# Kernel tuning notes

Measured on AMD Instinct MI355X. Metric: run time of the kernel, lower is better.

## Reference

```python
import jax, jax.numpy as jnp
import numpy as np

B, S, D_IN, HID, H = 4, 2048, 1024, 1024, 16
DH = HID // H


def setup_inputs() -> dict:
    key = jax.random.key(0)
    ks = jax.random.split(key, 10)
    s = 0.02
    return {
        "x": jax.random.normal(ks[0], (B, S, D_IN), dtype=jnp.float32),
        "Wq": jax.random.normal(ks[1], (D_IN, HID), dtype=jnp.float32) * s,
        "bq": jnp.zeros((HID,), dtype=jnp.float32),
        "Wk": jax.random.normal(ks[2], (D_IN, HID), dtype=jnp.float32) * s,
        "bk": jnp.zeros((HID,), dtype=jnp.float32),
        "Wv": jax.random.normal(ks[3], (D_IN, HID), dtype=jnp.float32) * s,
        "bv": jnp.zeros((HID,), dtype=jnp.float32),
        "Wo": jax.random.normal(ks[4], (HID, HID), dtype=jnp.float32) * s,
        "bo": jnp.zeros((HID,), dtype=jnp.float32),
        "padding_mask": jax.random.randint(ks[5], (B, S), 0, 2, dtype=jnp.int32),
    }


def reference(x, Wq, bq, Wk, bk, Wv, bv, Wo, bo, padding_mask):
    b, s, _ = x.shape
    q = (x @ Wq + bq).reshape(b, s, H, DH)  # [b, s, h, dh]
    k = (x @ Wk + bk).reshape(b, s, H, DH)
    v = (x @ Wv + bv).reshape(b, s, H, DH)

    # ALiBi: symmetric |i-j| distance bias, per-head slopes 2^{-m}
    r = jnp.arange(s)
    pos = jnp.abs(r[None, :] - r[:, None]).astype(jnp.float32)  # [s, s]
    step = 8.0 / H
    slopes = jnp.power(2.0, -jnp.arange(step, 8.0 + step, step, dtype=jnp.float32))  # [h]
    alibi = slopes[:, None, None] * pos[None, :, :]  # [h, s, s]

    scale = jnp.sqrt(jnp.float32(DH))
    attn = jnp.einsum("bqhd,bkhd->bhqk", q, k)
    attn = (attn - alibi[None]) / scale
    attn = jnp.where(padding_mask[:, None, None, :] == 0, -jnp.inf, attn)
    p = jax.nn.softmax(attn, axis=-1)

    out = jnp.einsum("bhqk,bkhd->bqhd", p, v).reshape(b, s, HID)
    return out @ Wo + bo
```

## Files before the change

### kernel.cpp

```cpp
#include <hip/hip_runtime.h>
#include <stdint.h>

#define NB     4
#define SEQ    2048
#define NH     16
#define DHD    64
#define DM     1024
#define MTOT   (NB*SEQ)

typedef __attribute__((ext_vector_type(8))) short bf16x8;
typedef __attribute__((ext_vector_type(4))) float f32x4;

__device__ __forceinline__ short f2bf(float f) {
  uint32_t u = __float_as_uint(f);
  u = (u + 0x7FFFu + ((u >> 16) & 1u)) >> 16;
  return (short)u;
}

__device__ __forceinline__ uint32_t cvtpk(float lo, float hi) {
  uint32_t r;
  asm("v_cvt_pk_bf16_f32 %0, %1, %2" : "=v"(r) : "v"(lo), "v"(hi));
  return r;
}

__device__ __forceinline__ float exp2a(float x) {
  float r;
  asm("v_exp_f32 %0, %1" : "=v"(r) : "v"(x));
  return r;
}

__device__ __forceinline__ float max3f(float a, float b, float c) {
  return fmaxf(fmaxf(a, b), c);
}

__device__ __forceinline__ f32x4 mfma16(bf16x8 a, bf16x8 b, f32x4 c) {
  return __builtin_amdgcn_mfma_f32_16x16x32_bf16(a, b, c, 0, 0, 0);
}

__device__ __forceinline__ void async16(const void* g, void* l) {
  __builtin_amdgcn_global_load_lds(
      (const __attribute__((address_space(1))) void*)g,
      (__attribute__((address_space(3))) void*)l, 16, 0, 0);
}

__global__ void k_cast(const float* __restrict__ in, short* __restrict__ out, int n) {
  int i = (blockIdx.x * blockDim.x + threadIdx.x) * 8;
  if (i >= n) return;
  float4 a = *reinterpret_cast<const float4*>(in + i);
  float4 b = *reinterpret_cast<const float4*>(in + i + 4);
  bf16x8 v;
  v[0] = f2bf(a.x); v[1] = f2bf(a.y); v[2] = f2bf(a.z); v[3] = f2bf(a.w);
  v[4] = f2bf(b.x); v[5] = f2bf(b.y); v[6] = f2bf(b.z); v[7] = f2bf(b.w);
  *reinterpret_cast<bf16x8*>(out + i) = v;
}

__global__ void k_maskbias(const int* __restrict__ pm, float* __restrict__ fb, int n) {
  int i = blockIdx.x * blockDim.x + threadIdx.x;
  if (i < n) fb[i] = pm[i] ? 0.0f : -1e30f;
}

__global__ void k_transpose(const float* __restrict__ in, short* __restrict__ out) {
  __shared__ float tile[32][33];
  int n0 = blockIdx.x * 32, k0 = blockIdx.y * 32;
  int tx = threadIdx.x, ty = threadIdx.y;
  #pragma unroll
  for (int i = 0; i < 32; i += 8)
    tile[ty + i][tx] = in[(size_t)(k0 + ty + i) * DM + n0 + tx];
  __syncthreads();
  #pragma unroll
  for (int i = 0; i < 32; i += 8)
    out[(size_t)(n0 + ty + i) * DM + k0 + tx] = f2bf(tile[tx][ty + i]);
}

template<int MODE>
__global__ void __launch_bounds__(256) k_gemm(const short* __restrict__ A,
                                              const short* __restrict__ Bt,
                                              const float* __restrict__ bias,
                                              void* __restrict__ Cv, float scale) {
  __shared__ short lA[128 * 32];
  __shared__ short lB[128 * 32];
  int lin = blockIdx.y * gridDim.x + blockIdx.x;
  int s = ((lin & 7) << 6) | (lin >> 3);
  int m0 = (s & 63) * 128, n0 = (s >> 6) * 128;
  int tid = threadIdx.x, lane = tid & 63, w = tid >> 6;
  int wr = w >> 1, wc = w & 1;
  int l15 = lane & 15, lg = lane >> 4;
  f32x4 acc[4][4] = {};

  int r0 = tid >> 2, c0 = (tid & 3) * 8;
  int r1 = (tid + 256) >> 2, c1 = ((tid + 256) & 3) * 8;
  const short* ga0 = A + (size_t)(m0 + r0) * DM + c0;
  const short* ga1 = A + (size_t)(m0 + r1) * DM + c1;
  const short* gb0 = Bt + (size_t)(n0 + r0) * DM + c0;
  const short* gb1 = Bt + (size_t)(n0 + r1) * DM + c1;
  short* lA0 = lA + w * 512;
  short* lA1 = lA + 2048 + w * 512;
  short* lB0 = lB + w * 512;
  short* lB1 = lB + 2048 + w * 512;

  for (int k0 = 0; k0 < DM; k0 += 32) {
    async16(ga0 + k0, lA0);
    async16(ga1 + k0, lA1);
    async16(gb0 + k0, lB0);
    async16(gb1 + k0, lB1);
    __syncthreads();
    bf16x8 af[4], bfr[4];
    #pragma unroll
    for (int i = 0; i < 4; ++i) {
      af[i]  = *reinterpret_cast<const bf16x8*>(lA + (wr * 64 + i * 16 + l15) * 32 + lg * 8);
      bfr[i] = *reinterpret_cast<const bf16x8*>(lB + (wc * 64 + i * 16 + l15) * 32 + lg * 8);
    }
    #pragma unroll
    for (int i = 0; i < 4; ++i)
      #pragma unroll
      for (int j = 0; j < 4; ++j)
        acc[i][j] = mfma16(af[i], bfr[j], acc[i][j]);
    __syncthreads();
  }

  #pragma unroll
  for (int j = 0; j < 4; ++j) {
    int cg = n0 + wc * 64 + j * 16 + l15;
    float bv = bias[cg];
    #pragma unroll
    for (int i = 0; i < 4; ++i) {
      #pragma unroll
      for (int r = 0; r < 4; ++r) {
        int rg = m0 + wr * 64 + i * 16 + lg * 4 + r;
        float val = (acc[i][j][r] + bv) * scale;
        if (MODE == 0)
          ((short*)Cv)[(size_t)rg * DM + cg] = f2bf(val);
        else if (MODE == 1)
          ((short*)Cv)[((size_t)((rg >> 11) * DM + cg)) * SEQ + (rg & 2047)] = f2bf(val);
        else
          ((float*)Cv)[(size_t)rg * DM + cg] = val;
      }
    }
  }
}

__device__ __forceinline__ void softmax_half(const f32x4* st, const float4* fb4,
                                             float c2, float d0, int lg,
                                             float& mrun, float& ssum,
                                             f32x4* acc, uint32_t* wb) {
  float l[16];
  #pragma unroll
  for (int t = 0; t < 4; ++t) {
    l[t * 4 + 0] = fmaf(-c2, fabsf(d0 - (float)(t * 16 + 0)), st[t][0] + fb4[t].x);
    l[t * 4 + 1] = fmaf(-c2, fabsf(d0 - (float)(t * 16 + 1)), st[t][1] + fb4[t].y);
    l[t * 4 + 2] = fmaf(-c2, fabsf(d0 - (float)(t * 16 + 2)), st[t][2] + fb4[t].z);
    l[t * 4 + 3] = fmaf(-c2, fabsf(d0 - (float)(t * 16 + 3)), st[t][3] + fb4[t].w);
  }
  float ma = max3f(l[0], l[1], l[2]);
  float mb = max3f(l[3], l[4], l[5]);
  float mc = max3f(l[6], l[7], l[8]);
  float md = max3f(l[9], l[10], l[11]);
  float me = max3f(l[12], l[13], l[14]);
  float tmax = fmaxf(max3f(ma, mb, mc), max3f(md, me, l[15]));
  tmax = fmaxf(tmax, __shfl_xor(tmax, 16));
  tmax = fmaxf(tmax, __shfl_xor(tmax, 32));

  if (!__all(tmax <= mrun + 8.0f)) {
    float mn = fmaxf(mrun, tmax);
    float fsc = exp2a(mrun - mn);
    mrun = mn;
    ssum *= fsc;
    #pragma unroll
    for (int td = 0; td < 4; ++td) acc[td] *= fsc;
  }

  float p[16];
  #pragma unroll
  for (int i = 0; i < 16; ++i) p[i] = exp2a(l[i] - mrun);
  float a0 = p[0] + p[1],  a1 = p[2] + p[3],  a2 = p[4] + p[5],  a3 = p[6] + p[7];
  float a4 = p[8] + p[9],  a5 = p[10] + p[11], a6 = p[12] + p[13], a7 = p[14] + p[15];
  float b0 = a0 + a1, b1 = a2 + a3, b2 = a4 + a5, b3 = a6 + a7;
  float rs = (b0 + b1) + (b2 + b3);
  rs += __shfl_xor(rs, 16);
  rs += __shfl_xor(rs, 32);
  ssum += rs;

  #pragma unroll
  for (int t = 0; t < 4; ++t) {
    uint2 wv = { cvtpk(p[t * 4 + 0], p[t * 4 + 1]), cvtpk(p[t * 4 + 2], p[t * 4 + 3]) };
    *reinterpret_cast<uint2*>(wb + t * 8 + lg * 2) = wv;
  }
}

__global__ void __launch_bounds__(256, 4) k_attn(const short* __restrict__ Q,
                                                 const short* __restrict__ Kb,
                                                 const short* __restrict__ Vt,
                                                 const float* __restrict__ fbias,
                                                 short* __restrict__ O) {
  __shared__ short lK[64 * 64];
  __shared__ short lV[64 * 64];
  __shared__ uint32_t pbuf[4 * 2 * 16 * 36];
  int qt = blockIdx.x, bh = blockIdx.y;
  int b = bh >> 4, h = bh & 15;
  int tid = threadIdx.x, lane = tid & 63, w = tid >> 6;
  int l15 = lane & 15, lg = lane >> 4;
  int q0 = qt * 128 + w * 32;
  float c2 = exp2f(-0.5f * (float)(h + 1)) * 0.125f * 1.44269504f;

  const short* qpA = Q + (size_t)(b * SEQ + q0 + l15) * DM + h * DHD + lg * 8;
  bf16x8 bqA0 = *reinterpret_cast<const bf16x8*>(qpA);
  bf16x8 bqA1 = *reinterpret_cast<const bf16x8*>(qpA + 32);
  const short* qpB = qpA + (size_t)16 * DM;
  bf16x8 bqB0 = *reinterpret_cast<const bf16x8*>(qpB);
  bf16x8 bqB1 = *reinterpret_cast<const bf16x8*>(qpB + 32);

  int srow0 = w * 8 + (lane >> 3);
  int srow1 = srow0 + 32;
  int sc0 = (lane & 7) ^ (srow0 & 7);
  int sc1 = (lane & 7) ^ (srow1 & 7);
  const short* kg0 = Kb + (size_t)(b * SEQ + srow0) * DM + h * DHD + sc0 * 8;
  const short* kg1 = Kb + (size_t)(b * SEQ + srow1) * DM + h * DHD + sc1 * 8;
  const short* vg0 = Vt + ((size_t)bh * DHD + srow0) * SEQ + sc0 * 8;
  const short* vg1 = Vt + ((size_t)bh * DHD + srow1) * SEQ + sc1 * 8;
  short* dK0 = lK + w * 512;
  short* dK1 = lK + 2048 + w * 512;
  short* dV0 = lV + w * 512;
  short* dV1 = lV + 2048 + w * 512;

  const float* fb = fbias + b * SEQ;
  uint32_t* wbA = pbuf + w * 1152 + l15 * 36;
  uint32_t* wbB = wbA + 576;
  int sw = l15 & 7;

  float mrunA = -1e30f, ssumA = 0.0f, mrunB = -1e30f, ssumB = 0.0f;
  f32x4 accA[4] = {}, accB[4] = {};
  float d0A = (float)(q0 + l15) - (float)(lg * 4);
  float d0B = d0A + 16.0f;

  for (int kt = 0; kt < SEQ; kt += 64) {
    async16(kg0, dK0);
    async16(kg1, dK1);
    async16(vg0, dV0);
    async16(vg1, dV1);
    kg0 += (size_t)64 * DM; kg1 += (size_t)64 * DM; vg0 += 64; vg1 += 64;

    float4 fb4[4];
    #pragma unroll
    for (int t = 0; t < 4; ++t)
      fb4[t] = *reinterpret_cast<const float4*>(fb + kt + t * 16 + lg * 4);

    __syncthreads();

    f32x4 stA[4], stB[4];
    __builtin_amdgcn_s_setprio(1);
    #pragma unroll
    for (int t = 0; t < 4; ++t) {
      int row = t * 16 + l15;
      bf16x8 k0 = *reinterpret_cast<const bf16x8*>(lK + row * 64 + (lg ^ sw) * 8);
      bf16x8 k1 = *reinterpret_cast<const bf16x8*>(lK + row * 64 + ((lg + 4) ^ sw) * 8);
      f32x4 zA = {};
      zA = mfma16(k0, bqA0, zA);
      stA[t] = mfma16(k1, bqA1, zA);
      f32x4 zB = {};
      zB = mfma16(k0, bqB0, zB);
      stB[t] = mfma16(k1, bqB1, zB);
    }
    __builtin_amdgcn_s_setprio(0);

    softmax_half(stA, fb4, c2, d0A, lg, mrunA, ssumA, accA, wbA);
    softmax_half(stB, fb4, c2, d0B, lg, mrunB, ssumB, accB, wbB);

    asm volatile("s_waitcnt lgkmcnt(0)" ::: "memory");
    __builtin_amdgcn_sched_barrier(0);

    __builtin_amdgcn_s_setprio(1);
    #pragma unroll
    for (int ks = 0; ks < 2; ++ks) {
      int t = ks * 2 + (lg >> 1);
      bf16x8 pfA = *reinterpret_cast<const bf16x8*>(wbA + t * 8 + (lg & 1) * 4);
      bf16x8 pfB = *reinterpret_cast<const bf16x8*>(wbB + t * 8 + (lg & 1) * 4);
      #pragma unroll
      for (int td = 0; td < 4; ++td) {
        int row = td * 16 + l15;
        bf16x8 vf = *reinterpret_cast<const bf16x8*>(lV + row * 64 + ((ks * 4 + lg) ^ sw) * 8);
        accA[td] = mfma16(vf, pfA, accA[td]);
        accB[td] = mfma16(vf, pfB, accB[td]);
      }
    }
    __builtin_amdgcn_s_setprio(0);
    d0A -= 64.0f; d0B -= 64.0f;
    __syncthreads();
  }

  float invA = 1.0f / ssumA;
  float invB = 1.0f / ssumB;
  short* opA = O + (size_t)(b * SEQ + q0 + l15) * DM + h * DHD;
  short* opB = opA + (size_t)16 * DM;
  #pragma unroll
  for (int td = 0; td < 4; ++td) {
    uint2 wvA = { cvtpk(accA[td][0] * invA, accA[td][1] * invA),
                  cvtpk(accA[td][2] * invA, accA[td][3] * invA) };
    *reinterpret_cast<uint2*>(opA + td * 16 + lg * 4) = wvA;
    uint2 wvB = { cvtpk(accB[td][0] * invB, accB[td][1] * invB),
                  cvtpk(accB[td][2] * invB, accB[td][3] * invB) };
    *reinterpret_cast<uint2*>(opB + td * 16 + lg * 4) = wvB;
  }
}

extern "C" void kernel_launch(void* const* d_in, const int* in_sizes, int n_in,
                              void* d_out, int out_size, void* d_ws, size_t ws_size,
                              hipStream_t stream) {
  const float* x  = (const float*)d_in[0];
  const float* Wq = (const float*)d_in[1];
  const float* bq = (const float*)d_in[2];
  const float* Wk = (const float*)d_in[3];
  const float* bk = (const float*)d_in[4];
  const float* Wv = (const float*)d_in[5];
  const float* bv = (const float*)d_in[6];
  const float* Wo = (const float*)d_in[7];
  const float* bo = (const float*)d_in[8];
  const int*   pm = (const int*)d_in[9];

  char* ws = (char*)d_ws;
  const size_t MB = 1ull << 20;
  short* xb  = (short*)(ws + 0 * MB);
  short* q   = (short*)(ws + 16 * MB);
  short* k   = (short*)(ws + 32 * MB);
  short* vt  = (short*)(ws + 48 * MB);
  short* ob  = (short*)(ws + 64 * MB);
  short* wqt = (short*)(ws + 80 * MB);
  short* wkt = (short*)(ws + 82 * MB);
  short* wvt = (short*)(ws + 84 * MB);
  short* wot = (short*)(ws + 86 * MB);
  float* fbias = (float*)(ws + 88 * MB);

  k_cast<<<dim3(MTOT * DM / 8 / 256), dim3(256), 0, stream>>>(x, xb, MTOT * DM);
  k_maskbias<<<dim3(MTOT / 256), dim3(256), 0, stream>>>(pm, fbias, MTOT);
  k_transpose<<<dim3(32, 32), dim3(32, 8), 0, stream>>>(Wq, wqt);
  k_transpose<<<dim3(32, 32), dim3(32, 8), 0, stream>>>(Wk, wkt);
  k_transpose<<<dim3(32, 32), dim3(32, 8), 0, stream>>>(Wv, wvt);
  k_transpose<<<dim3(32, 32), dim3(32, 8), 0, stream>>>(Wo, wot);
  k_gemm<0><<<dim3(64, 8), dim3(256), 0, stream>>>(xb, wqt, bq, q, 0.125f * 1.44269504f);
  k_gemm<0><<<dim3(64, 8), dim3(256), 0, stream>>>(xb, wkt, bk, k, 1.0f);
  k_gemm<1><<<dim3(64, 8), dim3(256), 0, stream>>>(xb, wvt, bv, vt, 1.0f);
  k_attn<<<dim3(SEQ / 128, NB * NH), dim3(256), 0, stream>>>(q, k, vt, fbias, ob);
  k_gemm<2><<<dim3(64, 8), dim3(256), 0, stream>>>(ob, wot, bo, d_out, 1.0f);
}
```

Baseline: 283.9 us.

## Register-prefetch next K/V tile during compute and remap attention grid for locality

```diff
diff --git a/kernel.cpp b/kernel.cpp
--- a/kernel.cpp
+++ b/kernel.cpp
@@ -195,7 +195,9 @@
   __shared__ short lK[64 * 64];
   __shared__ short lV[64 * 64];
   __shared__ uint32_t pbuf[4 * 2 * 16 * 36];
-  int qt = blockIdx.x, bh = blockIdx.y;
+  int g = blockIdx.x;
+  int qt = (g >> 3) & 15;
+  int bh = (g & 7) + ((g >> 7) << 3);
   int b = bh >> 4, h = bh & 15;
   int tid = threadIdx.x, lane = tid & 63, w = tid >> 6;
   int l15 = lane & 15, lg = lane >> 4;
@@ -209,18 +211,12 @@
   bf16x8 bqB0 = *reinterpret_cast<const bf16x8*>(qpB);
   bf16x8 bqB1 = *reinterpret_cast<const bf16x8*>(qpB + 32);
 
-  int srow0 = w * 8 + (lane >> 3);
-  int srow1 = srow0 + 32;
-  int sc0 = (lane & 7) ^ (srow0 & 7);
-  int sc1 = (lane & 7) ^ (srow1 & 7);
-  const short* kg0 = Kb + (size_t)(b * SEQ + srow0) * DM + h * DHD + sc0 * 8;
-  const short* kg1 = Kb + (size_t)(b * SEQ + srow1) * DM + h * DHD + sc1 * 8;
-  const short* vg0 = Vt + ((size_t)bh * DHD + srow0) * SEQ + sc0 * 8;
-  const short* vg1 = Vt + ((size_t)bh * DHD + srow1) * SEQ + sc1 * 8;
-  short* dK0 = lK + w * 512;
-  short* dK1 = lK + 2048 + w * 512;
-  short* dV0 = lV + w * 512;
-  short* dV1 = lV + 2048 + w * 512;
+  int srow = tid >> 3;
+  int scol = tid & 7;
+  const short* kgp = Kb + (size_t)(b * SEQ + srow) * DM + h * DHD + scol * 8;
+  const short* vgp = Vt + ((size_t)bh * DHD + srow) * SEQ + scol * 8;
+  int wofs = (scol ^ (srow & 7)) * 8;
+  int kw0 = srow * 64 + wofs, kw1 = kw0 + 32 * 64;
 
   const float* fb = fbias + b * SEQ;
   uint32_t* wbA = pbuf + w * 1152 + l15 * 36;
@@ -232,19 +228,31 @@
   float d0A = (float)(q0 + l15) - (float)(lg * 4);
   float d0B = d0A + 16.0f;
 
+  bf16x8 ks0 = *reinterpret_cast<const bf16x8*>(kgp);
+  bf16x8 ks1 = *reinterpret_cast<const bf16x8*>(kgp + (size_t)32 * DM);
+  bf16x8 vs0 = *reinterpret_cast<const bf16x8*>(vgp);
+  bf16x8 vs1 = *reinterpret_cast<const bf16x8*>(vgp + (size_t)32 * SEQ);
+  kgp += (size_t)64 * DM; vgp += 64;
+  *reinterpret_cast<bf16x8*>(lK + kw0) = ks0;
+  *reinterpret_cast<bf16x8*>(lK + kw1) = ks1;
+  *reinterpret_cast<bf16x8*>(lV + kw0) = vs0;
+  *reinterpret_cast<bf16x8*>(lV + kw1) = vs1;
+  __syncthreads();
+
   for (int kt = 0; kt < SEQ; kt += 64) {
-    async16(kg0, dK0);
-    async16(kg1, dK1);
-    async16(vg0, dV0);
-    async16(vg1, dV1);
-    kg0 += (size_t)64 * DM; kg1 += (size_t)64 * DM; vg0 += 64; vg1 += 64;
+    bool more = (kt + 64) < SEQ;
+    if (more) {
+      ks0 = *reinterpret_cast<const bf16x8*>(kgp);
+      ks1 = *reinterpret_cast<const bf16x8*>(kgp + (size_t)32 * DM);
+      vs0 = *reinterpret_cast<const bf16x8*>(vgp);
+      vs1 = *reinterpret_cast<const bf16x8*>(vgp + (size_t)32 * SEQ);
+      kgp += (size_t)64 * DM; vgp += 64;
+    }
 
     float4 fb4[4];
     #pragma unroll
     for (int t = 0; t < 4; ++t)
       fb4[t] = *reinterpret_cast<const float4*>(fb + kt + t * 16 + lg * 4);
-
-    __syncthreads();
 
     f32x4 stA[4], stB[4];
     __builtin_amdgcn_s_setprio(1);
@@ -284,6 +292,16 @@
     }
     __builtin_amdgcn_s_setprio(0);
     d0A -= 64.0f; d0B -= 64.0f;
+
+    __builtin_amdgcn_s_barrier();
+    __builtin_amdgcn_sched_barrier(0);
+    if (more) {
+      asm volatile("s_waitcnt vmcnt(0)" ::: "memory");
+      *reinterpret_cast<bf16x8*>(lK + kw0) = ks0;
+      *reinterpret_cast<bf16x8*>(lK + kw1) = ks1;
+      *reinterpret_cast<bf16x8*>(lV + kw0) = vs0;
+      *reinterpret_cast<bf16x8*>(lV + kw1) = vs1;
+    }
     __syncthreads();
   }
 
@@ -338,6 +356,6 @@
   k_gemm<0><<<dim3(64, 8), dim3(256), 0, stream>>>(xb, wqt, bq, q, 0.125f * 1.44269504f);
   k_gemm<0><<<dim3(64, 8), dim3(256), 0, stream>>>(xb, wkt, bk, k, 1.0f);
   k_gemm<1><<<dim3(64, 8), dim3(256), 0, stream>>>(xb, wvt, bv, vt, 1.0f);
-  k_attn<<<dim3(SEQ / 128, NB * NH), dim3(256), 0, stream>>>(q, k, vt, fbias, ob);
+  k_attn<<<dim3(SEQ / 128 * NB * NH), dim3(256), 0, stream>>>(q, k, vt, fbias, ob);
   k_gemm<2><<<dim3(64, 8), dim3(256), 0, stream>>>(ob, wot, bo, d_out, 1.0f);
 }
```

After: 317.1 us. 11.7% more time.

## Overlap K/V tile loads with compute via split async prefetch in attention

Applied to the files above, without the earlier changes.

```diff
diff --git a/kernel.cpp b/kernel.cpp
--- a/kernel.cpp
+++ b/kernel.cpp
@@ -187,15 +187,17 @@
   }
 }
 
-__global__ void __launch_bounds__(256, 4) k_attn(const short* __restrict__ Q,
-                                                 const short* __restrict__ Kb,
-                                                 const short* __restrict__ Vt,
-                                                 const float* __restrict__ fbias,
-                                                 short* __restrict__ O) {
+__global__ void __launch_bounds__(256) k_attn(const short* __restrict__ Q,
+                                              const short* __restrict__ Kb,
+                                              const short* __restrict__ Vt,
+                                              const float* __restrict__ fbias,
+                                              short* __restrict__ O) {
   __shared__ short lK[64 * 64];
   __shared__ short lV[64 * 64];
-  __shared__ uint32_t pbuf[4 * 2 * 16 * 36];
-  int qt = blockIdx.x, bh = blockIdx.y;
+  __shared__ uint32_t pbuf[4 * 2 * 16 * 38];
+  int g = blockIdx.x;
+  int qt = (g >> 3) & 15;
+  int bh = (g & 7) + ((g >> 7) << 3);
   int b = bh >> 4, h = bh & 15;
   int tid = threadIdx.x, lane = tid & 63, w = tid >> 6;
   int l15 = lane & 15, lg = lane >> 4;
@@ -223,8 +225,8 @@
   short* dV1 = lV + 2048 + w * 512;
 
   const float* fb = fbias + b * SEQ;
-  uint32_t* wbA = pbuf + w * 1152 + l15 * 36;
-  uint32_t* wbB = wbA + 576;
+  uint32_t* wbA = pbuf + w * 1216 + l15 * 38;
+  uint32_t* wbB = wbA + 608;
   int sw = l15 & 7;
 
   float mrunA = -1e30f, ssumA = 0.0f, mrunB = -1e30f, ssumB = 0.0f;
@@ -232,19 +234,24 @@
   float d0A = (float)(q0 + l15) - (float)(lg * 4);
   float d0B = d0A + 16.0f;
 
+  async16(kg0, dK0);
+  async16(kg1, dK1);
+  kg0 += (size_t)64 * DM; kg1 += (size_t)64 * DM;
+  async16(vg0, dV0);
+  async16(vg1, dV1);
+  vg0 += 64; vg1 += 64;
+
   for (int kt = 0; kt < SEQ; kt += 64) {
-    async16(kg0, dK0);
-    async16(kg1, dK1);
-    async16(vg0, dV0);
-    async16(vg1, dV1);
-    kg0 += (size_t)64 * DM; kg1 += (size_t)64 * DM; vg0 += 64; vg1 += 64;
+    bool more = (kt + 64) < SEQ;
+
+    asm volatile("s_waitcnt vmcnt(2)" ::: "memory");
+    __builtin_amdgcn_s_barrier();
+    __builtin_amdgcn_sched_barrier(0);
 
     float4 fb4[4];
     #pragma unroll
     for (int t = 0; t < 4; ++t)
       fb4[t] = *reinterpret_cast<const float4*>(fb + kt + t * 16 + lg * 4);
-
-    __syncthreads();
 
     f32x4 stA[4], stB[4];
     __builtin_amdgcn_s_setprio(1);
@@ -262,10 +269,23 @@
     }
     __builtin_amdgcn_s_setprio(0);
 
+    __builtin_amdgcn_s_barrier();
+    __builtin_amdgcn_sched_barrier(0);
+    if (more) {
+      async16(kg0, dK0);
+      async16(kg1, dK1);
+      kg0 += (size_t)64 * DM; kg1 += (size_t)64 * DM;
+    }
+
     softmax_half(stA, fb4, c2, d0A, lg, mrunA, ssumA, accA, wbA);
     softmax_half(stB, fb4, c2, d0B, lg, mrunB, ssumB, accB, wbB);
 
     asm volatile("s_waitcnt lgkmcnt(0)" ::: "memory");
+    if (more)
+      asm volatile("s_waitcnt vmcnt(2)" ::: "memory");
+    else
+      asm volatile("s_waitcnt vmcnt(0)" ::: "memory");
+    __builtin_amdgcn_s_barrier();
     __builtin_amdgcn_sched_barrier(0);
 
     __builtin_amdgcn_s_setprio(1);
@@ -284,7 +304,14 @@
     }
     __builtin_amdgcn_s_setprio(0);
     d0A -= 64.0f; d0B -= 64.0f;
-    __syncthreads();
+
+    __builtin_amdgcn_s_barrier();
+    __builtin_amdgcn_sched_barrier(0);
+    if (more) {
+      async16(vg0, dV0);
+      async16(vg1, dV1);
+      vg0 += 64; vg1 += 64;
+    }
   }
 
   float invA = 1.0f / ssumA;
@@ -338,6 +365,6 @@
   k_gemm<0><<<dim3(64, 8), dim3(256), 0, stream>>>(xb, wqt, bq, q, 0.125f * 1.44269504f);
   k_gemm<0><<<dim3(64, 8), dim3(256), 0, stream>>>(xb, wkt, bk, k, 1.0f);
   k_gemm<1><<<dim3(64, 8), dim3(256), 0, stream>>>(xb, wvt, bv, vt, 1.0f);
-  k_attn<<<dim3(SEQ / 128, NB * NH), dim3(256), 0, stream>>>(q, k, vt, fbias, ob);
+  k_attn<<<dim3(SEQ / 128 * NB * NH), dim3(256), 0, stream>>>(q, k, vt, fbias, ob);
   k_gemm<2><<<dim3(64, 8), dim3(256), 0, stream>>>(ob, wot, bo, d_out, 1.0f);
 }
```

After: 322.0 us. 13.4% more time.

## Prepack K/V in MFMA fragment order and load directly from global in single-wave attention

Applied to the files above, without the earlier changes.

```diff
diff --git a/kernel.cpp b/kernel.cpp
--- a/kernel.cpp
+++ b/kernel.cpp
@@ -7,6 +7,7 @@
 #define DHD    64
 #define DM     1024
 #define MTOT   (NB*SEQ)
+#define HSZ    (SEQ*DHD)
 
 typedef __attribute__((ext_vector_type(8))) short bf16x8;
 typedef __attribute__((ext_vector_type(4))) float f32x4;
@@ -128,12 +129,23 @@
       for (int r = 0; r < 4; ++r) {
         int rg = m0 + wr * 64 + i * 16 + lg * 4 + r;
         float val = (acc[i][j][r] + bv) * scale;
-        if (MODE == 0)
+        if (MODE == 0) {
           ((short*)Cv)[(size_t)rg * DM + cg] = f2bf(val);
-        else if (MODE == 1)
-          ((short*)Cv)[((size_t)((rg >> 11) * DM + cg)) * SEQ + (rg & 2047)] = f2bf(val);
-        else
+        } else if (MODE == 1) {
+          int bh2 = ((rg >> 11) << 4) | (cg >> 6);
+          int dh = cg & 63, sl = rg & 2047;
+          size_t fi = (size_t)bh2 * HSZ + (size_t)(sl >> 6) * 4096
+                    + (size_t)((((dh >> 4) * 8 + ((sl >> 3) & 7)) * 16 + (dh & 15)) * 8 + (sl & 7));
+          ((short*)Cv)[fi] = f2bf(val);
+        } else if (MODE == 3) {
+          int bh2 = ((rg >> 11) << 4) | (cg >> 6);
+          int dh = cg & 63, sl = rg & 2047;
+          size_t fi = (size_t)bh2 * HSZ + (size_t)(sl >> 4) * 1024
+                    + (size_t)((((dh >> 3) * 16 + (sl & 15)) * 8) + (dh & 7));
+          ((short*)Cv)[fi] = f2bf(val);
+        } else {
           ((float*)Cv)[(size_t)rg * DM + cg] = val;
+        }
       }
     }
   }
@@ -187,19 +199,19 @@
   }
 }
 
-__global__ void __launch_bounds__(256, 4) k_attn(const short* __restrict__ Q,
-                                                 const short* __restrict__ Kb,
-                                                 const short* __restrict__ Vt,
-                                                 const float* __restrict__ fbias,
-                                                 short* __restrict__ O) {
-  __shared__ short lK[64 * 64];
-  __shared__ short lV[64 * 64];
-  __shared__ uint32_t pbuf[4 * 2 * 16 * 36];
-  int qt = blockIdx.x, bh = blockIdx.y;
+__global__ void __launch_bounds__(64, 3) k_attn(const short* __restrict__ Q,
+                                                const short* __restrict__ KF,
+                                                const short* __restrict__ VF,
+                                                const float* __restrict__ fbias,
+                                                short* __restrict__ O) {
+  __shared__ uint32_t pbuf[2 * 16 * 38];
+  int g = blockIdx.x;
+  int qb = (g >> 3) & 63;
+  int bh = (g & 7) + ((g >> 9) << 3);
   int b = bh >> 4, h = bh & 15;
-  int tid = threadIdx.x, lane = tid & 63, w = tid >> 6;
+  int lane = threadIdx.x;
   int l15 = lane & 15, lg = lane >> 4;
-  int q0 = qt * 128 + w * 32;
+  int q0 = qb * 32;
   float c2 = exp2f(-0.5f * (float)(h + 1)) * 0.125f * 1.44269504f;
 
   const short* qpA = Q + (size_t)(b * SEQ + q0 + l15) * DM + h * DHD + lg * 8;
@@ -209,23 +221,11 @@
   bf16x8 bqB0 = *reinterpret_cast<const bf16x8*>(qpB);
   bf16x8 bqB1 = *reinterpret_cast<const bf16x8*>(qpB + 32);
 
-  int srow0 = w * 8 + (lane >> 3);
-  int srow1 = srow0 + 32;
-  int sc0 = (lane & 7) ^ (srow0 & 7);
-  int sc1 = (lane & 7) ^ (srow1 & 7);
-  const short* kg0 = Kb + (size_t)(b * SEQ + srow0) * DM + h * DHD + sc0 * 8;
-  const short* kg1 = Kb + (size_t)(b * SEQ + srow1) * DM + h * DHD + sc1 * 8;
-  const short* vg0 = Vt + ((size_t)bh * DHD + srow0) * SEQ + sc0 * 8;
-  const short* vg1 = Vt + ((size_t)bh * DHD + srow1) * SEQ + sc1 * 8;
-  short* dK0 = lK + w * 512;
-  short* dK1 = lK + 2048 + w * 512;
-  short* dV0 = lV + w * 512;
-  short* dV1 = lV + 2048 + w * 512;
-
+  const short* kbase = KF + (size_t)bh * HSZ + lane * 8;
+  const short* vbase = VF + (size_t)bh * HSZ + lane * 8;
   const float* fb = fbias + b * SEQ;
-  uint32_t* wbA = pbuf + w * 1152 + l15 * 36;
-  uint32_t* wbB = wbA + 576;
-  int sw = l15 & 7;
+  uint32_t* wbA = pbuf + l15 * 38;
+  uint32_t* wbB = pbuf + 608 + l15 * 38;
 
   float mrunA = -1e30f, ssumA = 0.0f, mrunB = -1e30f, ssumB = 0.0f;
   f32x4 accA[4] = {}, accB[4] = {};
@@ -233,32 +233,36 @@
   float d0B = d0A + 16.0f;
 
   for (int kt = 0; kt < SEQ; kt += 64) {
-    async16(kg0, dK0);
-    async16(kg1, dK1);
-    async16(vg0, dV0);
-    async16(vg1, dV1);
-    kg0 += (size_t)64 * DM; kg1 += (size_t)64 * DM; vg0 += 64; vg1 += 64;
-
     float4 fb4[4];
     #pragma unroll
     for (int t = 0; t < 4; ++t)
       fb4[t] = *reinterpret_cast<const float4*>(fb + kt + t * 16 + lg * 4);
 
-    __syncthreads();
+    const short* kp = kbase + (size_t)(kt >> 4) * 1024;
+    bf16x8 ka[4][2];
+    #pragma unroll
+    for (int t = 0; t < 4; ++t) {
+      ka[t][0] = *reinterpret_cast<const bf16x8*>(kp + t * 1024);
+      ka[t][1] = *reinterpret_cast<const bf16x8*>(kp + t * 1024 + 512);
+    }
+    const short* vp = vbase + (size_t)(kt >> 6) * 4096;
+    bf16x8 va[4][2];
+    #pragma unroll
+    for (int td = 0; td < 4; ++td) {
+      va[td][0] = *reinterpret_cast<const bf16x8*>(vp + (td * 8 + 0) * 128);
+      va[td][1] = *reinterpret_cast<const bf16x8*>(vp + (td * 8 + 4) * 128);
+    }
 
     f32x4 stA[4], stB[4];
     __builtin_amdgcn_s_setprio(1);
     #pragma unroll
     for (int t = 0; t < 4; ++t) {
-      int row = t * 16 + l15;
-      bf16x8 k0 = *reinterpret_cast<const bf16x8*>(lK + row * 64 + (lg ^ sw) * 8);
-      bf16x8 k1 = *reinterpret_cast<const bf16x8*>(lK + row * 64 + ((lg + 4) ^ sw) * 8);
       f32x4 zA = {};
-      zA = mfma16(k0, bqA0, zA);
-      stA[t] = mfma16(k1, bqA1, zA);
+      zA = mfma16(ka[t][0], bqA0, zA);
+      stA[t] = mfma16(ka[t][1], bqA1, zA);
       f32x4 zB = {};
-      zB = mfma16(k0, bqB0, zB);
-      stB[t] = mfma16(k1, bqB1, zB);
+      zB = mfma16(ka[t][0], bqB0, zB);
+      stB[t] = mfma16(ka[t][1], bqB1, zB);
     }
     __builtin_amdgcn_s_setprio(0);
 
@@ -276,15 +280,12 @@
       bf16x8 pfB = *reinterpret_cast<const bf16x8*>(wbB + t * 8 + (lg & 1) * 4);
       #pragma unroll
       for (int td = 0; td < 4; ++td) {
-        int row = td * 16 + l15;
-        bf16x8 vf = *reinterpret_cast<const bf16x8*>(lV + row * 64 + ((ks * 4 + lg) ^ sw) * 8);
-        accA[td] = mfma16(vf, pfA, accA[td]);
-        accB[td] = mfma16(vf, pfB, accB[td]);
+        accA[td] = mfma16(va[td][ks], pfA, accA[td]);
+        accB[td] = mfma16(va[td][ks], pfB, accB[td]);
       }
     }
     __builtin_amdgcn_s_setprio(0);
     d0A -= 64.0f; d0B -= 64.0f;
-    __syncthreads();
   }
 
   float invA = 1.0f / ssumA;
@@ -320,8 +321,8 @@
   const size_t MB = 1ull << 20;
   short* xb  = (short*)(ws + 0 * MB);
   short* q   = (short*)(ws + 16 * MB);
-  short* k   = (short*)(ws + 32 * MB);
-  short* vt  = (short*)(ws + 48 * MB);
+  short* kf  = (short*)(ws + 32 * MB);
+  short* vf  = (short*)(ws + 48 * MB);
   short* ob  = (short*)(ws + 64 * MB);
   short* wqt = (short*)(ws + 80 * MB);
   short* wkt = (short*)(ws + 82 * MB);
@@ -336,8 +337,8 @@
   k_transpose<<<dim3(32, 32), dim3(32, 8), 0, stream>>>(Wv, wvt);
   k_transpose<<<dim3(32, 32), dim3(32, 8), 0, stream>>>(Wo, wot);
   k_gemm<0><<<dim3(64, 8), dim3(256), 0, stream>>>(xb, wqt, bq, q, 0.125f * 1.44269504f);
-  k_gemm<0><<<dim3(64, 8), dim3(256), 0, stream>>>(xb, wkt, bk, k, 1.0f);
-  k_gemm<1><<<dim3(64, 8), dim3(256), 0, stream>>>(xb, wvt, bv, vt, 1.0f);
-  k_attn<<<dim3(SEQ / 128, NB * NH), dim3(256), 0, stream>>>(q, k, vt, fbias, ob);
+  k_gemm<3><<<dim3(64, 8), dim3(256), 0, stream>>>(xb, wkt, bk, kf, 1.0f);
+  k_gemm<1><<<dim3(64, 8), dim3(256), 0, stream>>>(xb, wvt, bv, vf, 1.0f);
+  k_attn<<<dim3(SEQ / 32 * NB * NH), dim3(64), 0, stream>>>(q, kf, vf, fbias, ob);
   k_gemm<2><<<dim3(64, 8), dim3(256), 0, stream>>>(ob, wot, bo, d_out, 1.0f);
 }
```

Result: faster. 260.0 us (-8.4%).
